# Kernel tuning notes

Measured on AMD Instinct MI355X. Metric: run time of the kernel, lower is better.

## Reference

```python
import jax, jax.numpy as jnp
import numpy as np

N_HEADS, N_KV, HEAD_DIM = 32, 8, 128
N_REP = N_HEADS // N_KV
THETA = 500000.0
EPS = 1e-5


def _rope_vectors(cache_len, dtype):
    half = HEAD_DIM // 2
    freqs = 1.0 / (THETA ** (np.arange(half, dtype=np.float64) / HEAD_DIM))
    ang = cache_len * freqs
    cos = np.concatenate([np.cos(ang), np.cos(ang)])
    sin = np.concatenate([-np.sin(ang), np.sin(ang)])
    return jnp.asarray(cos, dtype), jnp.asarray(sin, dtype)


def setup_inputs() -> dict:
    key = jax.random.key(0)
    ks = jax.random.split(key, 8)
    B, H, L = 128, 4096, 1024
    w_scale = 0.02  # keep logits in a sane range
    return {
        "x": jax.random.normal(ks[0], (B, 1, H), jnp.float32),
        "k_cache": jax.random.normal(ks[1], (B, N_KV, L, HEAD_DIM), jnp.float32),
        "v_cache": jax.random.normal(ks[2], (B, N_KV, L, HEAD_DIM), jnp.float32),
        "norm_w": jnp.ones((H,), jnp.float32),
        "wq": jax.random.normal(ks[3], (H, N_HEADS * HEAD_DIM), jnp.float32) * w_scale,
        "wk": jax.random.normal(ks[4], (H, N_KV * HEAD_DIM), jnp.float32) * w_scale,
        "wv": jax.random.normal(ks[5], (H, N_KV * HEAD_DIM), jnp.float32) * w_scale,
        "wo": jax.random.normal(ks[6], (N_HEADS * HEAD_DIM, H), jnp.float32) * w_scale,
    }


def reference(x, k_cache, v_cache, norm_w, wq, wk, wv, wo):
    B = x.shape[0]
    L = k_cache.shape[2]
    rope_cos, rope_sin = _rope_vectors(L, x.dtype)

    # RMSNorm
    xn = x * jax.lax.rsqrt(jnp.mean(x * x, axis=-1, keepdims=True) + EPS) * norm_w

    # Projections (seq len is 1, so fold it away)
    q = (xn @ wq).reshape(B, N_KV, N_REP, HEAD_DIM)   # (b, g, r, d)
    k_new = (xn @ wk).reshape(B, N_KV, HEAD_DIM)       # (b, g, d)
    v_new = (xn @ wv).reshape(B, N_KV, HEAD_DIM)

    # Module's simplified "RoPE": x*cos + x*sin (no rotate_half)
    rope = rope_cos + rope_sin
    q = q * rope
    k_new = k_new * rope

    scale = 1.0 / (HEAD_DIM ** 0.5)

    # Attention over cached K/V (GQA: rep queries share one kv head)
    cache_scores = jnp.einsum("bgrd,bgld->bgrl", q, k_cache) * scale
    cache_probs = jax.nn.softmax(cache_scores, axis=-1)
    cache_out = jnp.einsum("bgrl,bgld->bgrd", cache_probs, v_cache)

    # Separate attention term for the new token (softmax over a length-1 axis)
    new_scores = jnp.einsum("bgrd,bgd->bgr", q, k_new) * scale
    new_probs = jax.nn.softmax(new_scores[..., None], axis=-1)  # == 1.0
    new_out = new_probs * v_new[:, :, None, :]                  # (b, g, r, d)

    out = (cache_out + new_out).reshape(B, 1, N_HEADS * HEAD_DIM)
    return out @ wo
```

## Files before the change

### kernel.cpp

```cpp
#include <hip/hip_runtime.h>
#include <math.h>


#define THREADS 256

__global__ __launch_bounds__(256) void rmsnorm_kernel(
    const float* __restrict__ x, const float* __restrict__ w,
    float* __restrict__ xn, int H) {
  int b = blockIdx.x;
  int t = threadIdx.x;
  const float4* x4 = (const float4*)(x + (size_t)b * H);
  const float4* w4 = (const float4*)w;
  float4* y4 = (float4*)(xn + (size_t)b * H);
  int n4 = H >> 2;
  float ss = 0.f;
  for (int i = t; i < n4; i += THREADS) {
    float4 v = x4[i];
    ss += v.x * v.x + v.y * v.y + v.z * v.z + v.w * v.w;
  }
#pragma unroll
  for (int off = 32; off; off >>= 1) ss += __shfl_xor(ss, off, 64);
  __shared__ float red[4];
  if ((t & 63) == 0) red[t >> 6] = ss;
  __syncthreads();
  float tot = red[0] + red[1] + red[2] + red[3];
  float rs = rsqrtf(tot / (float)H + 1e-5f);
  for (int i = t; i < n4; i += THREADS) {
    float4 v = x4[i];
    float4 g = w4[i];
    float4 o;
    o.x = v.x * rs * g.x;
    o.y = v.y * rs * g.y;
    o.z = v.z * rs * g.z;
    o.w = v.w * rs * g.w;
    y4[i] = o;
  }
}

__global__ void rope_kernel(float* __restrict__ rope, int L) {
  int d = threadIdx.x;
  int i = d & 63;
  double ang = (double)L * pow(500000.0, -((double)i) / 128.0);
  double c = cos(ang), s = sin(ang);
  rope[d] = (float)(d < 64 ? c - s : c + s);
}

__global__ __launch_bounds__(256) void gemm32(
    const float* __restrict__ X, int K,
    const float* __restrict__ W1, int n1,
    const float* __restrict__ W2, int n2,
    const float* __restrict__ rope,
    float* __restrict__ Y1, float* __restrict__ Y2) {
  __shared__ float xs[32][36];
  __shared__ float wsh[32][36];
  int t = threadIdx.x;
  int colOff = blockIdx.x * 32;
  int rowOff = blockIdx.y * 32;
  bool reg2 = (colOff >= n1);
  const float* W = reg2 ? W2 : W1;
  int ld = reg2 ? n2 : n1;
  int c0 = reg2 ? colOff - n1 : colOff;
  int lr = t >> 3;
  int lc4 = t & 7;
  float4 acc = make_float4(0.f, 0.f, 0.f, 0.f);
  for (int kc = 0; kc < K; kc += 32) {
    float4 xv = *(const float4*)(X + (size_t)(rowOff + lr) * K + kc + lc4 * 4);
    float4 wv = *(const float4*)(W + (size_t)(kc + lr) * ld + c0 + lc4 * 4);
    xs[lr][lc4 * 4 + 0] = xv.x;
    xs[lr][lc4 * 4 + 1] = xv.y;
    xs[lr][lc4 * 4 + 2] = xv.z;
    xs[lr][lc4 * 4 + 3] = xv.w;
    *(float4*)(&wsh[lr][lc4 * 4]) = wv;
    __syncthreads();
#pragma unroll
    for (int k = 0; k < 32; k += 4) {
      float4 xq = *(const float4*)(&xs[lr][k]);
#pragma unroll
      for (int kk = 0; kk < 4; kk++) {
        float4 wq4 = *(const float4*)(&wsh[k + kk][lc4 * 4]);
        float xsc = (&xq.x)[kk];
        acc.x += xsc * wq4.x;
        acc.y += xsc * wq4.y;
        acc.z += xsc * wq4.z;
        acc.w += xsc * wq4.w;
      }
    }
    __syncthreads();
  }
  float4 o = acc;
  if (!reg2 && rope != nullptr) {
    float4 rp = *(const float4*)(rope + ((colOff + lc4 * 4) & 127));
    o.x *= rp.x;
    o.y *= rp.y;
    o.z *= rp.z;
    o.w *= rp.w;
  }
  float* Y = reg2 ? Y2 : Y1;
  *(float4*)(Y + (size_t)(rowOff + lr) * ld + c0 + lc4 * 4) = o;
}

__global__ __launch_bounds__(256) void attn_kernel(
    const float* __restrict__ q, const float* __restrict__ kc_,
    const float* __restrict__ vc_, const float* __restrict__ vnew,
    float* __restrict__ ho, int L) {
  __shared__ float sK[64][132];
  __shared__ float sS[4][1024];
  __shared__ float sQ[4][128];
  int t = threadIdx.x;
  int b = blockIdx.x >> 3;
  int g = blockIdx.x & 7;
  for (int i = t; i < 512; i += 256) {
    int r = i >> 7, d = i & 127;
    sQ[r][d] = q[(size_t)b * 4096 + (size_t)(g * 4 + r) * 128 + d];
  }
  __syncthreads();
  int r = t >> 6;
  int l = t & 63;
  const float scale = 0.08838834764831845f;
  int ntiles = L >> 6;
  const float* kbase = kc_ + (size_t)(b * 8 + g) * (size_t)L * 128;
  for (int tile = 0; tile < ntiles; tile++) {
    const float* src = kbase + (size_t)tile * 64 * 128;
#pragma unroll
    for (int i = 0; i < 8; i++) {
      int id = t + 256 * i;
      int lr = id >> 5, c4 = id & 31;
      float4 v = *(const float4*)(src + (size_t)lr * 128 + c4 * 4);
      *(float4*)(&sK[lr][c4 * 4]) = v;
    }
    __syncthreads();
    float4 a = make_float4(0.f, 0.f, 0.f, 0.f);
#pragma unroll
    for (int c4 = 0; c4 < 32; c4++) {
      float4 kv = *(const float4*)(&sK[l][c4 * 4]);
      float4 qv = *(const float4*)(&sQ[r][c4 * 4]);
      a.x += kv.x * qv.x;
      a.y += kv.y * qv.y;
      a.z += kv.z * qv.z;
      a.w += kv.w * qv.w;
    }
    sS[r][tile * 64 + l] = (a.x + a.y + a.z + a.w) * scale;
    __syncthreads();
  }
  float m = -INFINITY;
  for (int i = 0; i < ntiles; i++) m = fmaxf(m, sS[r][l + 64 * i]);
#pragma unroll
  for (int off = 32; off; off >>= 1) m = fmaxf(m, __shfl_xor(m, off, 64));
  float sum = 0.f;
  for (int i = 0; i < ntiles; i++) {
    float e = __expf(sS[r][l + 64 * i] - m);
    sS[r][l + 64 * i] = e;
    sum += e;
  }
#pragma unroll
  for (int off = 32; off; off >>= 1) sum += __shfl_xor(sum, off, 64);
  float inv = 1.f / sum;
  for (int i = 0; i < ntiles; i++) sS[r][l + 64 * i] *= inv;
  __syncthreads();
  int d0 = l * 2;
  float acc0 = 0.f, acc1 = 0.f;
  const float* vbase = vc_ + (size_t)(b * 8 + g) * (size_t)L * 128;
  for (int tile = 0; tile < ntiles; tile++) {
    const float* src = vbase + (size_t)tile * 64 * 128;
#pragma unroll
    for (int i = 0; i < 8; i++) {
      int id = t + 256 * i;
      int lr = id >> 5, c4 = id & 31;
      float4 v = *(const float4*)(src + (size_t)lr * 128 + c4 * 4);
      *(float4*)(&sK[lr][c4 * 4]) = v;
    }
    __syncthreads();
#pragma unroll
    for (int ll = 0; ll < 64; ll++) {
      float p = sS[r][tile * 64 + ll];
      float2 v = *(const float2*)(&sK[ll][d0]);
      acc0 += p * v.x;
      acc1 += p * v.y;
    }
    __syncthreads();
  }
  float2 vn = *(const float2*)(vnew + (size_t)b * 1024 + (size_t)g * 128 + d0);
  float2 o;
  o.x = acc0 + vn.x;
  o.y = acc1 + vn.y;
  *(float2*)(ho + (size_t)b * 4096 + (size_t)(g * 4 + r) * 128 + d0) = o;
}

extern "C" void kernel_launch(void* const* d_in, const int* in_sizes, int n_in,
                              void* d_out, int out_size, void* d_ws, size_t ws_size,
                              hipStream_t stream) {
  const float* x = (const float*)d_in[0];
  const float* kcache = (const float*)d_in[1];
  const float* vcache = (const float*)d_in[2];
  const float* normw = (const float*)d_in[3];
  const float* wq = (const float*)d_in[4];
  const float* wv = (const float*)d_in[6];
  const float* wo = (const float*)d_in[7];
  float* out = (float*)d_out;

  int H = in_sizes[3];
  int B = in_sizes[0] / H;
  int Dq = in_sizes[4] / H;
  int Dv = in_sizes[6] / H;
  long long L = (long long)in_sizes[1] / ((long long)B * Dv);

  float* xn = (float*)d_ws;
  float* rope = xn + (size_t)B * H;
  float* qws = rope + 128;
  float* vnew = qws + (size_t)B * Dq;
  float* ho = vnew + (size_t)B * Dv;

  rmsnorm_kernel<<<B, 256, 0, stream>>>(x, normw, xn, H);
  rope_kernel<<<1, 128, 0, stream>>>(rope, (int)L);
  gemm32<<<dim3((Dq + Dv) / 32, B / 32), 256, 0, stream>>>(
      xn, H, wq, Dq, wv, Dv, rope, qws, vnew);
  attn_kernel<<<B * 8, 256, 0, stream>>>(qws, kcache, vcache, vnew, ho, (int)L);
  gemm32<<<dim3(H / 32, B / 32), 256, 0, stream>>>(
      ho, Dq, wo, H, nullptr, 0, nullptr, out, nullptr);
}
```

Measured before the change: 1.396 ms.

## Stream K/V from global directly into registers in attention, drop LDS staging

The attention kernel no longer stages K and V tiles through shared memory with block-wide barriers. Q is held in registers, and each 8-lane group computes dot products for one key, reduced with shuffles. The PV phase has each wave read V rows straight from global memory. This is meant to remove LDS traffic and per-tile syncs, and to expose more memory-level parallelism on a bandwidth-bound cache scan. The cost is heavier register use and redundant V reads across the four waves, which are expected to hit in cache.

Result: no change. 1.388 ms (-0.6%).

```diff
diff --git a/kernel.cpp b/kernel.cpp
--- a/kernel.cpp
+++ b/kernel.cpp
@@ -103,81 +103,106 @@
     const float* __restrict__ q, const float* __restrict__ kc_,
     const float* __restrict__ vc_, const float* __restrict__ vnew,
     float* __restrict__ ho, int L) {
-  __shared__ float sK[64][132];
   __shared__ float sS[4][1024];
-  __shared__ float sQ[4][128];
   int t = threadIdx.x;
   int b = blockIdx.x >> 3;
   int g = blockIdx.x & 7;
-  for (int i = t; i < 512; i += 256) {
-    int r = i >> 7, d = i & 127;
-    sQ[r][d] = q[(size_t)b * 4096 + (size_t)(g * 4 + r) * 128 + d];
+  int w = t >> 6;
+  int l = t & 63;
+  int li = l & 7;
+  int kg = l >> 3;
+  const float scale = 0.08838834764831845f;
+
+  const float* qbase = q + (size_t)b * 4096 + (size_t)g * 512;
+  float4 qf[4][4];
+#pragma unroll
+  for (int r = 0; r < 4; r++)
+#pragma unroll
+    for (int j = 0; j < 4; j++)
+      qf[r][j] = *(const float4*)(qbase + r * 128 + li * 4 + j * 32);
+
+  const float* kbase = kc_ + (size_t)(b * 8 + g) * (size_t)L * 128;
+  int nIter = L >> 5;
+#pragma unroll 2
+  for (int it = 0; it < nIter; ++it) {
+    int key = it * 32 + w * 8 + kg;
+    const float4* kp = (const float4*)(kbase + (size_t)key * 128);
+    float4 k0 = kp[li];
+    float4 k1 = kp[li + 8];
+    float4 k2 = kp[li + 16];
+    float4 k3 = kp[li + 24];
+    float s0, s1, s2, s3;
+    {
+      float4 a = qf[0][0], bq = qf[0][1], c = qf[0][2], d = qf[0][3];
+      s0 = k0.x * a.x + k0.y * a.y + k0.z * a.z + k0.w * a.w
+         + k1.x * bq.x + k1.y * bq.y + k1.z * bq.z + k1.w * bq.w
+         + k2.x * c.x + k2.y * c.y + k2.z * c.z + k2.w * c.w
+         + k3.x * d.x + k3.y * d.y + k3.z * d.z + k3.w * d.w;
+    }
+    {
+      float4 a = qf[1][0], bq = qf[1][1], c = qf[1][2], d = qf[1][3];
+      s1 = k0.x * a.x + k0.y * a.y + k0.z * a.z + k0.w * a.w
+         + k1.x * bq.x + k1.y * bq.y + k1.z * bq.z + k1.w * bq.w
+         + k2.x * c.x + k2.y * c.y + k2.z * c.z + k2.w * c.w
+         + k3.x * d.x + k3.y * d.y + k3.z * d.z + k3.w * d.w;
+    }
+    {
+      float4 a = qf[2][0], bq = qf[2][1], c = qf[2][2], d = qf[2][3];
+      s2 = k0.x * a.x + k0.y * a.y + k0.z * a.z + k0.w * a.w
+         + k1.x * bq.x + k1.y * bq.y + k1.z * bq.z + k1.w * bq.w
+         + k2.x * c.x + k2.y * c.y + k2.z * c.z + k2.w * c.w
+         + k3.x * d.x + k3.y * d.y + k3.z * d.z + k3.w * d.w;
+    }
+    {
+      float4 a = qf[3][0], bq = qf[3][1], c = qf[3][2], d = qf[3][3];
+      s3 = k0.x * a.x + k0.y * a.y + k0.z * a.z + k0.w * a.w
+         + k1.x * bq.x + k1.y * bq.y + k1.z * bq.z + k1.w * bq.w
+         + k2.x * c.x + k2.y * c.y + k2.z * c.z + k2.w * c.w
+         + k3.x * d.x + k3.y * d.y + k3.z * d.z + k3.w * d.w;
+    }
+#pragma unroll
+    for (int off = 1; off < 8; off <<= 1) {
+      s0 += __shfl_xor(s0, off, 64);
+      s1 += __shfl_xor(s1, off, 64);
+      s2 += __shfl_xor(s2, off, 64);
+      s3 += __shfl_xor(s3, off, 64);
+    }
+    if (li == 0)      sS[0][key] = s0 * scale;
+    else if (li == 1) sS[1][key] = s1 * scale;
+    else if (li == 2) sS[2][key] = s2 * scale;
+    else if (li == 3) sS[3][key] = s3 * scale;
   }
   __syncthreads();
-  int r = t >> 6;
-  int l = t & 63;
-  const float scale = 0.08838834764831845f;
-  int ntiles = L >> 6;
-  const float* kbase = kc_ + (size_t)(b * 8 + g) * (size_t)L * 128;
-  for (int tile = 0; tile < ntiles; tile++) {
-    const float* src = kbase + (size_t)tile * 64 * 128;
-#pragma unroll
-    for (int i = 0; i < 8; i++) {
-      int id = t + 256 * i;
-      int lr = id >> 5, c4 = id & 31;
-      float4 v = *(const float4*)(src + (size_t)lr * 128 + c4 * 4);
-      *(float4*)(&sK[lr][c4 * 4]) = v;
-    }
-    __syncthreads();
-    float4 a = make_float4(0.f, 0.f, 0.f, 0.f);
-#pragma unroll
-    for (int c4 = 0; c4 < 32; c4++) {
-      float4 kv = *(const float4*)(&sK[l][c4 * 4]);
-      float4 qv = *(const float4*)(&sQ[r][c4 * 4]);
-      a.x += kv.x * qv.x;
-      a.y += kv.y * qv.y;
-      a.z += kv.z * qv.z;
-      a.w += kv.w * qv.w;
-    }
-    sS[r][tile * 64 + l] = (a.x + a.y + a.z + a.w) * scale;
-    __syncthreads();
-  }
+
+  int r = w;
   float m = -INFINITY;
-  for (int i = 0; i < ntiles; i++) m = fmaxf(m, sS[r][l + 64 * i]);
+  for (int i = l; i < L; i += 64) m = fmaxf(m, sS[r][i]);
 #pragma unroll
   for (int off = 32; off; off >>= 1) m = fmaxf(m, __shfl_xor(m, off, 64));
   float sum = 0.f;
-  for (int i = 0; i < ntiles; i++) {
-    float e = __expf(sS[r][l + 64 * i] - m);
-    sS[r][l + 64 * i] = e;
+  for (int i = l; i < L; i += 64) {
+    float e = __expf(sS[r][i] - m);
+    sS[r][i] = e;
     sum += e;
   }
 #pragma unroll
   for (int off = 32; off; off >>= 1) sum += __shfl_xor(sum, off, 64);
   float inv = 1.f / sum;
-  for (int i = 0; i < ntiles; i++) sS[r][l + 64 * i] *= inv;
-  __syncthreads();
+  for (int i = l; i < L; i += 64) sS[r][i] *= inv;
+
   int d0 = l * 2;
   float acc0 = 0.f, acc1 = 0.f;
   const float* vbase = vc_ + (size_t)(b * 8 + g) * (size_t)L * 128;
-  for (int tile = 0; tile < ntiles; tile++) {
-    const float* src = vbase + (size_t)tile * 64 * 128;
-#pragma unroll
-    for (int i = 0; i < 8; i++) {
-      int id = t + 256 * i;
-      int lr = id >> 5, c4 = id & 31;
-      float4 v = *(const float4*)(src + (size_t)lr * 128 + c4 * 4);
-      *(float4*)(&sK[lr][c4 * 4]) = v;
-    }
-    __syncthreads();
-#pragma unroll
-    for (int ll = 0; ll < 64; ll++) {
-      float p = sS[r][tile * 64 + ll];
-      float2 v = *(const float2*)(&sK[ll][d0]);
-      acc0 += p * v.x;
-      acc1 += p * v.y;
-    }
-    __syncthreads();
+#pragma unroll 4
+  for (int ll4 = 0; ll4 < L; ll4 += 4) {
+    float4 p4 = *(const float4*)(&sS[r][ll4]);
+    const float* v0 = vbase + (size_t)ll4 * 128 + d0;
+    float2 va = *(const float2*)(v0);
+    float2 vb = *(const float2*)(v0 + 128);
+    float2 vc2 = *(const float2*)(v0 + 256);
+    float2 vd = *(const float2*)(v0 + 384);
+    acc0 += p4.x * va.x + p4.y * vb.x + p4.z * vc2.x + p4.w * vd.x;
+    acc1 += p4.x * va.y + p4.y * vb.y + p4.z * vc2.y + p4.w * vd.y;
   }
   float2 vn = *(const float2*)(vnew + (size_t)b * 1024 + (size_t)g * 128 + d0);
   float2 o;
```
